# Kernel optimization log

Measured on AMD Instinct MI355X. Metric: run time of the kernel, lower is better.

The kernel has to match this reference:

```python
import jax, jax.numpy as jnp
import numpy as np


def rgb_to_hue(rgb):
    # rgb: [B,3,H,W] -> hue in [0,1), shape [B,1,H,W]
    cmax = jnp.max(rgb, axis=1, keepdims=True)
    cmin = jnp.min(rgb, axis=1, keepdims=True)
    cmax_idx = jnp.argmax(rgb, axis=1, keepdims=True)  # first max, like torch.max
    delta = cmax - cmin
    cmax_idx = jnp.where(delta == 0, 3, cmax_idx)      # achromatic -> branch 3 (hue 0)
    safe_delta = jnp.where(delta == 0, 1.0, delta)     # avoid div-by-zero; masked out below
    r, g, b = rgb[:, 0:1], rgb[:, 1:2], rgb[:, 2:3]
    h0 = jnp.mod((g - b) / safe_delta, 6.0)
    h1 = (b - r) / safe_delta + 2.0
    h2 = (r - g) / safe_delta + 4.0
    hue = jnp.where(cmax_idx == 0, h0,
          jnp.where(cmax_idx == 1, h1,
          jnp.where(cmax_idx == 2, h2, 0.0)))
    return hue / 6.0


def setup_inputs() -> dict:
    key = jax.random.key(0)
    k1, k2, k3 = jax.random.split(key, 3)
    x = jax.random.uniform(k1, (32, 3, 512, 512), dtype=jnp.float32)
    W = jax.random.normal(k2, (1, 1, 1, 1), dtype=jnp.float32)  # Conv2d(1,1,k=1) weight
    b = jax.random.normal(k3, (1,), dtype=jnp.float32)          # Conv2d bias
    return {"x": x, "W": W, "b": b}


def reference(x, W, b):
    hue = rgb_to_hue(x)                 # [B,1,H,W]
    # 1x1 conv with 1 in / 1 out channel == scalar scale + bias
    out = hue * W[0, 0, 0, 0] + b[0]    # [B,1,H,W]
    return out
```

## Files before the change

### kernel.cpp

```cpp
#include <hip/hip_runtime.h>


#define HW    262144
#define NPIX  8388608

__global__ __launch_bounds__(256) void HBEMD_F_67156108640795_kernel(
    const float* __restrict__ x,
    const float* __restrict__ Wp,
    const float* __restrict__ Bp,
    float* __restrict__ out)
{
    int v = blockIdx.x * blockDim.x + threadIdx.x;
    int o = v << 2;
    if (o >= NPIX) return;

    int n = o >> 18;
    int p = o & (HW - 1);
    const float* base = x + (size_t)n * (3 * HW) + p;

    float4 r4 = *(const float4*)(base);
    float4 g4 = *(const float4*)(base + HW);
    float4 b4 = *(const float4*)(base + 2 * HW);

    float w  = Wp[0];
    float bb = Bp[0];

    float rr[4] = {r4.x, r4.y, r4.z, r4.w};
    float gg[4] = {g4.x, g4.y, g4.z, g4.w};
    float bl[4] = {b4.x, b4.y, b4.z, b4.w};
    float oo[4];

#pragma unroll
    for (int k = 0; k < 4; ++k) {
        float r = rr[k], g = gg[k], b = bl[k];
        float cmax  = fmaxf(r, fmaxf(g, b));
        float cmin  = fminf(r, fminf(g, b));
        float delta = cmax - cmin;

        float sd  = (delta == 0.0f) ? 1.0f : delta;
        float inv = 1.0f / sd;

        float t0 = (g - b) * inv;
        t0 = (t0 < 0.0f) ? (t0 + 6.0f) : t0;
        float t1 = (b - r) * inv + 2.0f;
        float t2 = (r - g) * inv + 4.0f;

        float hue = (r == cmax) ? t0 : ((g == cmax) ? t1 : t2);
        hue = (delta == 0.0f) ? 0.0f : hue;

        oo[k] = (hue / 6.0f) * w + bb;
    }

    float4 o4 = make_float4(oo[0], oo[1], oo[2], oo[3]);
    *(float4*)(out + o) = o4;
}

extern "C" void kernel_launch(void* const* d_in, const int* in_sizes, int n_in,
                              void* d_out, int out_size, void* d_ws, size_t ws_size,
                              hipStream_t stream) {
    const float* x  = (const float*)d_in[0];
    const float* W  = (const float*)d_in[1];
    const float* b  = (const float*)d_in[2];
    float* out = (float*)d_out;

    const int threads = 256;
    const int nvec = NPIX / 4;
    const int blocks = nvec / threads;
    HBEMD_F_67156108640795_kernel<<<blocks, threads, 0, stream>>>(x, W, b, out);
}
```

Baseline: 155.4 us.

## Process eight pixels per thread with nontemporal loads/stores and fast reciprocal

Each thread now handles eight pixels through two float4 loads per channel, and the grid is halved to match. Loads and stores use nontemporal builtins to avoid polluting the cache on a pure streaming pass. The exact division is replaced by the hardware approximate reciprocal. The divide by six is folded into the weight, and the scale and bias are applied with FMA. Small numeric differences can appear from the approximate reciprocal and the folded 1/6.

New measurement: 154.8 us. About the same (-0.4%).

```diff
diff --git a/kernel.cpp b/kernel.cpp
--- a/kernel.cpp
+++ b/kernel.cpp
@@ -3,6 +3,27 @@
 
 #define HW    262144
 #define NPIX  8388608
+
+typedef float f4 __attribute__((ext_vector_type(4)));
+
+__device__ __forceinline__ float hue_px(float r, float g, float b,
+                                        float w6, float bb) {
+    float cmax  = fmaxf(r, fmaxf(g, b));
+    float cmin  = fminf(r, fminf(g, b));
+    float delta = cmax - cmin;
+
+    float inv = __builtin_amdgcn_rcpf(delta);
+
+    float t0 = (g - b) * inv;
+    t0 = (t0 < 0.0f) ? (t0 + 6.0f) : t0;
+    float t1 = fmaf(b - r, inv, 2.0f);
+    float t2 = fmaf(r - g, inv, 4.0f);
+
+    float hue = (r == cmax) ? t0 : ((g == cmax) ? t1 : t2);
+    hue = (delta == 0.0f) ? 0.0f : hue;
+
+    return fmaf(hue, w6, bb);
+}
 
 __global__ __launch_bounds__(256) void HBEMD_F_67156108640795_kernel(
     const float* __restrict__ x,
@@ -11,48 +32,32 @@
     float* __restrict__ out)
 {
     int v = blockIdx.x * blockDim.x + threadIdx.x;
-    int o = v << 2;
+    int o = v << 3;
     if (o >= NPIX) return;
 
     int n = o >> 18;
     int p = o & (HW - 1);
     const float* base = x + (size_t)n * (3 * HW) + p;
 
-    float4 r4 = *(const float4*)(base);
-    float4 g4 = *(const float4*)(base + HW);
-    float4 b4 = *(const float4*)(base + 2 * HW);
+    f4 r0 = __builtin_nontemporal_load((const f4*)(base));
+    f4 r1 = __builtin_nontemporal_load((const f4*)(base + 4));
+    f4 g0 = __builtin_nontemporal_load((const f4*)(base + HW));
+    f4 g1 = __builtin_nontemporal_load((const f4*)(base + HW + 4));
+    f4 b0 = __builtin_nontemporal_load((const f4*)(base + 2 * HW));
+    f4 b1 = __builtin_nontemporal_load((const f4*)(base + 2 * HW + 4));
 
-    float w  = Wp[0];
+    float w6 = Wp[0] * 0.16666667f;
     float bb = Bp[0];
 
-    float rr[4] = {r4.x, r4.y, r4.z, r4.w};
-    float gg[4] = {g4.x, g4.y, g4.z, g4.w};
-    float bl[4] = {b4.x, b4.y, b4.z, b4.w};
-    float oo[4];
-
+    f4 o0, o1;
 #pragma unroll
     for (int k = 0; k < 4; ++k) {
-        float r = rr[k], g = gg[k], b = bl[k];
-        float cmax  = fmaxf(r, fmaxf(g, b));
-        float cmin  = fminf(r, fminf(g, b));
-        float delta = cmax - cmin;
-
-        float sd  = (delta == 0.0f) ? 1.0f : delta;
-        float inv = 1.0f / sd;
-
-        float t0 = (g - b) * inv;
-        t0 = (t0 < 0.0f) ? (t0 + 6.0f) : t0;
-        float t1 = (b - r) * inv + 2.0f;
-        float t2 = (r - g) * inv + 4.0f;
-
-        float hue = (r == cmax) ? t0 : ((g == cmax) ? t1 : t2);
-        hue = (delta == 0.0f) ? 0.0f : hue;
-
-        oo[k] = (hue / 6.0f) * w + bb;
+        o0[k] = hue_px(r0[k], g0[k], b0[k], w6, bb);
+        o1[k] = hue_px(r1[k], g1[k], b1[k], w6, bb);
     }
 
-    float4 o4 = make_float4(oo[0], oo[1], oo[2], oo[3]);
-    *(float4*)(out + o) = o4;
+    __builtin_nontemporal_store(o0, (f4*)(out + o));
+    __builtin_nontemporal_store(o1, (f4*)(out + o + 4));
 }
 
 extern "C" void kernel_launch(void* const* d_in, const int* in_sizes, int n_in,
@@ -64,7 +69,7 @@
     float* out = (float*)d_out;
 
     const int threads = 256;
-    const int nvec = NPIX / 4;
-    const int blocks = nvec / threads;
+    const int ngrp = NPIX / 8;
+    const int blocks = ngrp / threads;
     HBEMD_F_67156108640795_kernel<<<blocks, threads, 0, stream>>>(x, W, b, out);
 }
```
